# Optimization experiments

Hardware: AMD Instinct MI355X
Metric: run time of the kernel (lower is better)

The kernel has to match this reference:

```python
import jax, jax.numpy as jnp
import numpy as np

U, I, H, E = 50000, 50000, 128, 800000


def segment_softmax(vals, seg, num):
    m = jax.ops.segment_max(vals, seg, num_segments=num)
    ex = jnp.exp(vals - m[seg])
    s = jax.ops.segment_sum(ex, seg, num_segments=num)
    return ex / s[seg]


def setup_inputs() -> dict:
    key = jax.random.key(0)
    ks = jax.random.split(key, 16)
    scale = 1.0 / np.sqrt(H)
    inp = {
        "u_emb": jax.random.normal(ks[0], (U, H), jnp.float32),
        "i_emb": jax.random.normal(ks[1], (I, H), jnp.float32),
        "pVui": jax.random.normal(ks[2], (E, H), jnp.float32),
        "pKiu": jax.random.normal(ks[3], (E, H), jnp.float32),
        "w1": jax.random.normal(ks[4], (H, H), jnp.float32) * scale,
        "w2": jax.random.normal(ks[5], (H, H), jnp.float32) * scale,
        "w1b": jax.random.normal(ks[6], (H, H), jnp.float32) * scale,
        "w2b": jax.random.normal(ks[7], (H, H), jnp.float32) * scale,
        "w3": jax.random.normal(ks[8], (H, H), jnp.float32) * scale,
        "w4": jax.random.normal(ks[9], (H, H), jnp.float32) * scale,
        "edge_index": jax.random.randint(ks[10], (2, E), 0, min(U, I), jnp.int64),
        "last_u": jax.random.randint(ks[11], (2, U), 0, I, jnp.int64),
        "last_i": jax.random.randint(ks[12], (2, I), 0, U, jnp.int64),
        "graph": jnp.zeros((1,), jnp.int64),
    }
    return inp


def reference(u_emb, i_emb, pVui, pKiu, w1, w2, w1b, w2b, w3, w4,
              edge_index, last_u, last_i, graph):
    sqrt_d = np.sqrt(float(u_emb.shape[1])).astype if False else float(np.sqrt(u_emb.shape[1]))
    nu, ni = u_emb.shape[0], i_emb.shape[0]
    src_u, dst_i = edge_index[0], edge_index[1]  # per-edge (user, item)

    # ---- longterm ----
    um_att = u_emb @ w2.T            # [U,H]
    im_att = i_emb @ w1.T            # [I,H]
    # sparse_dense_mul(edge_index, um_att @ im_att.T) -> per-edge dot products
    e_vals = jnp.sum(um_att[src_u] * im_att[dst_i], axis=-1)  # [E]
    e_ui = e_vals + jnp.sum(um_att[src_u] * pVui, axis=-1)
    alphas = segment_softmax(e_ui / sqrt_d, src_u, nu)        # softmax over items per user
    e_iu = e_vals + jnp.sum(im_att[dst_i] * pKiu, axis=-1)
    betas = segment_softmax(e_iu / sqrt_d, dst_i, ni)         # softmax over users per item
    um_b = u_emb @ w2b.T
    im_b = i_emb @ w1b.T
    hLu = jax.ops.segment_sum(alphas[:, None] * (im_b[dst_i] + pKiu), src_u, num_segments=nu)
    hLi = jax.ops.segment_sum(betas[:, None] * (um_b[src_u] + pVui), dst_i, num_segments=ni)

    # ---- shortterm ----
    last_item = i_emb[last_u[1]] @ w3.T   # [U,H] last item embedding per user
    last_user = u_emb[last_i[1]] @ w4.T   # [I,H] last user embedding per item
    a_vals = jnp.sum(last_item[src_u] * im_att[dst_i], axis=-1)
    s_alphas = segment_softmax(a_vals / sqrt_d, src_u, nu)
    b_vals = jnp.sum(last_user[src_u] * im_att[dst_i], axis=-1)
    s_betas = segment_softmax(b_vals / sqrt_d, dst_i, ni)
    # pass_messages with p = ones -> messages + 1
    hSu = jax.ops.segment_sum(s_alphas[:, None] * (im_att[dst_i] + 1.0), src_u, num_segments=nu)
    hSi = jax.ops.segment_sum(s_betas[:, None] * (um_att[src_u] + 1.0), dst_i, num_segments=ni)
    return (hLu, hSu, hLi, hSi)
```

## Files before the change

### kernel.cpp

```cpp
#include <hip/hip_runtime.h>
#include <hip/hip_bf16.h>
#include <math.h>


#define WB 1024

typedef float fvec4 __attribute__((ext_vector_type(4)));

__device__ __forceinline__ float4 nt_load4(const float* p) {
    fvec4 v = __builtin_nontemporal_load((const fvec4*)p);
    return make_float4(v.x, v.y, v.z, v.w);
}
__device__ __forceinline__ float dot4(float4 a, float4 b) {
    return a.x * b.x + a.y * b.y + a.z * b.z + a.w * b.w;
}

struct Gemm6Desc {
    const float* X[6];
    const float* W[6];
    float*       O[6];
    const int*   g[6];
    int          ostride[6];
    int          nrows[6];
};

__global__ __launch_bounds__(256) void gemm6_kernel(Gemm6Desc d)
{
    __shared__ float Xl[64 * 32];
    __shared__ float Wl[128 * 32];
    const int j6 = blockIdx.y;
    const float* __restrict__ X = d.X[j6];
    const float* __restrict__ W = d.W[j6];
    float* __restrict__ O       = d.O[j6];
    const int* __restrict__ gidx = d.g[j6];
    const int ostride = d.ostride[j6];
    const int nrows   = d.nrows[j6];

    const int t  = threadIdx.x;
    const int tx = t & 15;
    const int ty = t >> 4;
    const int brow = blockIdx.x * 64;
    if (brow >= nrows) return;

    float acc[4][8];
#pragma unroll
    for (int j = 0; j < 4; ++j)
#pragma unroll
        for (int i = 0; i < 8; ++i) acc[j][i] = 0.f;

    for (int k0 = 0; k0 < 128; k0 += 32) {
        __syncthreads();
#pragma unroll
        for (int u = 0; u < 2; ++u) {
            int idx4 = t + u * 256;
            int r  = idx4 >> 3;
            int k4 = idx4 & 7;
            int row = brow + r;
            float4 v = make_float4(0.f, 0.f, 0.f, 0.f);
            if (row < nrows) {
                int g = gidx ? gidx[row] : row;
                v = *(const float4*)(X + (size_t)g * 128 + k0 + k4 * 4);
            }
            int sw = k4 ^ ((r >> 3) & 7);
            *(float4*)(Xl + r * 32 + sw * 4) = v;
        }
#pragma unroll
        for (int u = 0; u < 4; ++u) {
            int idx4 = t + u * 256;
            int c  = idx4 >> 3;
            int k4 = idx4 & 7;
            float4 v = *(const float4*)(W + (size_t)c * 128 + k0 + k4 * 4);
            int sw = k4 ^ ((c >> 3) & 7);
            *(float4*)(Wl + c * 32 + sw * 4) = v;
        }
        __syncthreads();
#pragma unroll
        for (int k4 = 0; k4 < 8; ++k4) {
            float4 xv[4], wv[8];
#pragma unroll
            for (int j = 0; j < 4; ++j) {
                int r = ty * 4 + j;
                xv[j] = *(const float4*)(Xl + r * 32 + ((k4 ^ ((r >> 3) & 7)) * 4));
            }
#pragma unroll
            for (int i = 0; i < 8; ++i) {
                int c = tx * 8 + i;
                wv[i] = *(const float4*)(Wl + c * 32 + ((k4 ^ ((c >> 3) & 7)) * 4));
            }
#pragma unroll
            for (int j = 0; j < 4; ++j)
#pragma unroll
                for (int i = 0; i < 8; ++i) {
                    acc[j][i] += xv[j].x * wv[i].x;
                    acc[j][i] += xv[j].y * wv[i].y;
                    acc[j][i] += xv[j].z * wv[i].z;
                    acc[j][i] += xv[j].w * wv[i].w;
                }
        }
    }
#pragma unroll
    for (int j = 0; j < 4; ++j) {
        int row = brow + ty * 4 + j;
        if (row < nrows) {
            float* op = O + (size_t)row * ostride + tx * 8;
            *(float4*)(op)     = make_float4(acc[j][0], acc[j][1], acc[j][2], acc[j][3]);
            *(float4*)(op + 4) = make_float4(acc[j][4], acc[j][5], acc[j][6], acc[j][7]);
        }
    }
}

__global__ __launch_bounds__(256) void hist_kernel(
    const int* __restrict__ ei, int E,
    int* __restrict__ deg_u, int* __restrict__ deg_i)
{
    int e = blockIdx.x * 256 + threadIdx.x;
    if (e < E) {
        atomicAdd(&deg_u[ei[e]], 1);
        atomicAdd(&deg_i[ei[E + e]], 1);
    }
}

__global__ __launch_bounds__(256) void scan_blocksums_kernel(
    const int* __restrict__ deg_u, int nu, int nbu,
    const int* __restrict__ deg_i, int ni,
    int* __restrict__ bsum)
{
    int b = blockIdx.x;
    const int* deg; int n; int base;
    if (b < nbu) { deg = deg_u; n = nu; base = b * WB; }
    else         { deg = deg_i; n = ni; base = (b - nbu) * WB; }
    int t = threadIdx.x;
    int s = 0;
#pragma unroll
    for (int j = 0; j < 4; ++j) {
        int i = base + t * 4 + j;
        if (i < n) s += deg[i];
    }
#pragma unroll
    for (int o = 32; o > 0; o >>= 1) s += __shfl_xor(s, o);
    __shared__ int wt[4];
    if ((t & 63) == 0) wt[t >> 6] = s;
    __syncthreads();
    if (t == 0) bsum[b] = wt[0] + wt[1] + wt[2] + wt[3];
}

__global__ void scan_partials_kernel(
    const int* __restrict__ bsum, int* __restrict__ bscan,
    int nbu, int nbi,
    int* __restrict__ off_u, int nu, int* __restrict__ off_i, int ni)
{
    if (threadIdx.x != 0) return;
    if (blockIdx.x == 0) {
        int c = 0;
        for (int b = 0; b < nbu; ++b) { bscan[b] = c; c += bsum[b]; }
        off_u[nu] = c;
    } else {
        int c = 0;
        for (int b = 0; b < nbi; ++b) { bscan[nbu + b] = c; c += bsum[nbu + b]; }
        off_i[ni] = c;
    }
}

__global__ __launch_bounds__(256) void scan_final_kernel(
    const int* __restrict__ deg_u, int nu, int nbu,
    const int* __restrict__ deg_i, int ni,
    const int* __restrict__ bscan,
    int* __restrict__ off_u, int* __restrict__ cur_u,
    int* __restrict__ off_i, int* __restrict__ cur_i)
{
    int b = blockIdx.x;
    const int* deg; int n; int base; int* off; int* cur;
    if (b < nbu) { deg = deg_u; n = nu; base = b * WB; off = off_u; cur = cur_u; }
    else         { deg = deg_i; n = ni; base = (b - nbu) * WB; off = off_i; cur = cur_i; }
    int t = threadIdx.x;
    int lane = t & 63, w = t >> 6;
    int v[4];
    int s = 0;
#pragma unroll
    for (int j = 0; j < 4; ++j) {
        int i = base + t * 4 + j;
        v[j] = (i < n) ? deg[i] : 0;
        s += v[j];
    }
    int inc = s;
#pragma unroll
    for (int o = 1; o < 64; o <<= 1) {
        int x = __shfl_up(inc, o);
        if (lane >= o) inc += x;
    }
    int excl = inc - s;
    __shared__ int wt[4];
    if (lane == 63) wt[w] = inc;
    __syncthreads();
    int wbase = 0;
    for (int j = 0; j < w; ++j) wbase += wt[j];
    int e = bscan[b] + wbase + excl;
#pragma unroll
    for (int j = 0; j < 4; ++j) {
        int i = base + t * 4 + j;
        if (i < n) { off[i] = e; cur[i] = e; }
        e += v[j];
    }
}

__global__ __launch_bounds__(256) void scatter_ids_kernel(
    const int* __restrict__ ei, int E,
    int* __restrict__ cur_u, int* __restrict__ cur_i,
    int* __restrict__ eu_list, int* __restrict__ ei_list)
{
    int e = blockIdx.x * 256 + threadIdx.x;
    if (e < E) {
        int pu = atomicAdd(&cur_u[ei[e]], 1);
        eu_list[pu] = e;
        int pi = atomicAdd(&cur_i[ei[E + e]], 1);
        ei_list[pi] = e;
    }
}

__global__ __launch_bounds__(256) void gather_u_kernel(
    const float* __restrict__ fusedU,
    const float* __restrict__ fusedI,
    const float* __restrict__ last_item, const float* __restrict__ last_user,
    const float* __restrict__ pVui, const float* __restrict__ pKiu,
    const int* __restrict__ ei, int E,
    const int* __restrict__ off_u, const int* __restrict__ eu_list,
    float2* __restrict__ x24,
    float* __restrict__ hLu, float* __restrict__ hSu, int U, float inv_sqrt_d)
{
    const int wid  = (int)(((size_t)blockIdx.x * blockDim.x + threadIdx.x) >> 6);
    const int lane = threadIdx.x & 63;
    if (wid >= U) return;
    const int g = lane >> 4;
    const int q = lane & 15;

    const float4* fu4 = (const float4*)(fusedU    + (size_t)wid * 256);
    const float4* li4 = (const float4*)(last_item + (size_t)wid * 128);
    const float4* lu4 = (const float4*)(last_user + (size_t)wid * 128);
    const float4 um0 = fu4[q],      um1 = fu4[q + 16];
    const float4 li0 = li4[q],      li1 = li4[q + 16];
    const float4 lu0 = lu4[q],      lu1 = lu4[q + 16];

    float4 a1l = make_float4(0.f,0.f,0.f,0.f), a1h = make_float4(0.f,0.f,0.f,0.f);
    float4 a3l = make_float4(0.f,0.f,0.f,0.f), a3h = make_float4(0.f,0.f,0.f,0.f);
    float s1 = 0.f, s3 = 0.f;
    const int e0 = off_u[wid], e1 = off_u[wid + 1];
    for (int e = e0 + g; e < e1; e += 4) {
        const int eid = eu_list[e];
        const int dst = ei[E + eid];
        const float4* fI = (const float4*)(fusedI + (size_t)dst * 256);
        const float* pvp = pVui + (size_t)eid * 128;
        const float* pkp = pKiu + (size_t)eid * 128;
        float4 ia0 = fI[q],      ia1 = fI[q + 16];
        float4 ib0 = fI[32 + q], ib1 = fI[48 + q];
        float4 pv0 = nt_load4(pvp + q * 4), pv1 = nt_load4(pvp + 64 + q * 4);
        float4 pk0 = nt_load4(pkp + q * 4), pk1 = nt_load4(pkp + 64 + q * 4);

        float p0 = dot4(um0, ia0) + dot4(um1, ia1);
        float p1 = dot4(um0, pv0) + dot4(um1, pv1);
        float p2 = dot4(ia0, pk0) + dot4(ia1, pk1);
        float q1 = p0 + p1;
        float q2 = p0 + p2;
        float q3 = dot4(li0, ia0) + dot4(li1, ia1);
        float q4 = dot4(lu0, ia0) + dot4(lu1, ia1);
#pragma unroll
        for (int o = 8; o > 0; o >>= 1) {
            q1 += __shfl_xor(q1, o);
            q2 += __shfl_xor(q2, o);
            q3 += __shfl_xor(q3, o);
            q4 += __shfl_xor(q4, o);
        }
        float x1 = __expf(q1 * inv_sqrt_d);
        float x2 = __expf(q2 * inv_sqrt_d);
        float x3 = __expf(q3 * inv_sqrt_d);
        float x4 = __expf(q4 * inv_sqrt_d);
        a1l.x += x1*(ib0.x+pk0.x); a1l.y += x1*(ib0.y+pk0.y);
        a1l.z += x1*(ib0.z+pk0.z); a1l.w += x1*(ib0.w+pk0.w);
        a1h.x += x1*(ib1.x+pk1.x); a1h.y += x1*(ib1.y+pk1.y);
        a1h.z += x1*(ib1.z+pk1.z); a1h.w += x1*(ib1.w+pk1.w);
        a3l.x += x3*(ia0.x+1.f);   a3l.y += x3*(ia0.y+1.f);
        a3l.z += x3*(ia0.z+1.f);   a3l.w += x3*(ia0.w+1.f);
        a3h.x += x3*(ia1.x+1.f);   a3h.y += x3*(ia1.y+1.f);
        a3h.z += x3*(ia1.z+1.f);   a3h.w += x3*(ia1.w+1.f);
        s1 += x1; s3 += x3;
        if (q == 0) x24[eid] = make_float2(x2, x4);
    }
#pragma unroll
    for (int o = 16; o <= 32; o <<= 1) {
        a1l.x += __shfl_xor(a1l.x, o); a1l.y += __shfl_xor(a1l.y, o);
        a1l.z += __shfl_xor(a1l.z, o); a1l.w += __shfl_xor(a1l.w, o);
        a1h.x += __shfl_xor(a1h.x, o); a1h.y += __shfl_xor(a1h.y, o);
        a1h.z += __shfl_xor(a1h.z, o); a1h.w += __shfl_xor(a1h.w, o);
        a3l.x += __shfl_xor(a3l.x, o); a3l.y += __shfl_xor(a3l.y, o);
        a3l.z += __shfl_xor(a3l.z, o); a3l.w += __shfl_xor(a3l.w, o);
        a3h.x += __shfl_xor(a3h.x, o); a3h.y += __shfl_xor(a3h.y, o);
        a3h.z += __shfl_xor(a3h.z, o); a3h.w += __shfl_xor(a3h.w, o);
        s1 += __shfl_xor(s1, o);       s3 += __shfl_xor(s3, o);
    }
    if (lane < 16) {
        float r1 = (s1 > 0.f) ? 1.f / s1 : 0.f;
        float r3 = (s3 > 0.f) ? 1.f / s3 : 0.f;
        float4* oL = (float4*)(hLu + (size_t)wid * 128);
        float4* oS = (float4*)(hSu + (size_t)wid * 128);
        oL[q]      = make_float4(a1l.x*r1, a1l.y*r1, a1l.z*r1, a1l.w*r1);
        oL[q + 16] = make_float4(a1h.x*r1, a1h.y*r1, a1h.z*r1, a1h.w*r1);
        oS[q]      = make_float4(a3l.x*r3, a3l.y*r3, a3l.z*r3, a3l.w*r3);
        oS[q + 16] = make_float4(a3h.x*r3, a3h.y*r3, a3h.z*r3, a3h.w*r3);
    }
}

__global__ __launch_bounds__(256) void gather_i_kernel(
    const float* __restrict__ fusedU,
    const float* __restrict__ pVui,
    const int* __restrict__ ei, int E,
    const int* __restrict__ off_i, const int* __restrict__ ei_list,
    const float2* __restrict__ x24,
    float* __restrict__ hLi, float* __restrict__ hSi, int I)
{
    const int wid  = (int)(((size_t)blockIdx.x * blockDim.x + threadIdx.x) >> 6);
    const int lane = threadIdx.x & 63;
    if (wid >= I) return;
    const int g = lane >> 4;
    const int q = lane & 15;

    float4 a2l = make_float4(0.f,0.f,0.f,0.f), a2h = make_float4(0.f,0.f,0.f,0.f);
    float4 a4l = make_float4(0.f,0.f,0.f,0.f), a4h = make_float4(0.f,0.f,0.f,0.f);
    float s2 = 0.f, s4 = 0.f;
    const int e0 = off_i[wid], e1 = off_i[wid + 1];
    for (int e = e0 + g; e < e1; e += 4) {
        const int eid = ei_list[e];
        const int src = ei[eid];
        const float2 x = x24[eid];
        const float4* fU = (const float4*)(fusedU + (size_t)src * 256);
        const float* pvp = pVui + (size_t)eid * 128;
        float4 ua0 = fU[q],      ua1 = fU[q + 16];
        float4 ub0 = fU[32 + q], ub1 = fU[48 + q];
        float4 pv0 = nt_load4(pvp + q * 4), pv1 = nt_load4(pvp + 64 + q * 4);
        a2l.x += x.x*(ub0.x+pv0.x); a2l.y += x.x*(ub0.y+pv0.y);
        a2l.z += x.x*(ub0.z+pv0.z); a2l.w += x.x*(ub0.w+pv0.w);
        a2h.x += x.x*(ub1.x+pv1.x); a2h.y += x.x*(ub1.y+pv1.y);
        a2h.z += x.x*(ub1.z+pv1.z); a2h.w += x.x*(ub1.w+pv1.w);
        a4l.x += x.y*(ua0.x+1.f);   a4l.y += x.y*(ua0.y+1.f);
        a4l.z += x.y*(ua0.z+1.f);   a4l.w += x.y*(ua0.w+1.f);
        a4h.x += x.y*(ua1.x+1.f);   a4h.y += x.y*(ua1.y+1.f);
        a4h.z += x.y*(ua1.z+1.f);   a4h.w += x.y*(ua1.w+1.f);
        s2 += x.x; s4 += x.y;
    }
#pragma unroll
    for (int o = 16; o <= 32; o <<= 1) {
        a2l.x += __shfl_xor(a2l.x, o); a2l.y += __shfl_xor(a2l.y, o);
        a2l.z += __shfl_xor(a2l.z, o); a2l.w += __shfl_xor(a2l.w, o);
        a2h.x += __shfl_xor(a2h.x, o); a2h.y += __shfl_xor(a2h.y, o);
        a2h.z += __shfl_xor(a2h.z, o); a2h.w += __shfl_xor(a2h.w, o);
        a4l.x += __shfl_xor(a4l.x, o); a4l.y += __shfl_xor(a4l.y, o);
        a4l.z += __shfl_xor(a4l.z, o); a4l.w += __shfl_xor(a4l.w, o);
        a4h.x += __shfl_xor(a4h.x, o); a4h.y += __shfl_xor(a4h.y, o);
        a4h.z += __shfl_xor(a4h.z, o); a4h.w += __shfl_xor(a4h.w, o);
        s2 += __shfl_xor(s2, o);       s4 += __shfl_xor(s4, o);
    }
    if (lane < 16) {
        float r2 = (s2 > 0.f) ? 1.f / s2 : 0.f;
        float r4 = (s4 > 0.f) ? 1.f / s4 : 0.f;
        float4* oL = (float4*)(hLi + (size_t)wid * 128);
        float4* oS = (float4*)(hSi + (size_t)wid * 128);
        oL[q]      = make_float4(a2l.x*r2, a2l.y*r2, a2l.z*r2, a2l.w*r2);
        oL[q + 16] = make_float4(a2h.x*r2, a2h.y*r2, a2h.z*r2, a2h.w*r2);
        oS[q]      = make_float4(a4l.x*r4, a4l.y*r4, a4l.z*r4, a4l.w*r4);
        oS[q + 16] = make_float4(a4h.x*r4, a4h.y*r4, a4h.z*r4, a4h.w*r4);
    }
}

extern "C" void kernel_launch(void* const* d_in, const int* in_sizes, int n_in,
                              void* d_out, int out_size, void* d_ws, size_t ws_size,
                              hipStream_t stream)
{
    const float* u_emb = (const float*)d_in[0];
    const float* i_emb = (const float*)d_in[1];
    const float* pVui  = (const float*)d_in[2];
    const float* pKiu  = (const float*)d_in[3];
    const float* w1    = (const float*)d_in[4];
    const float* w2    = (const float*)d_in[5];
    const float* w1b   = (const float*)d_in[6];
    const float* w2b   = (const float*)d_in[7];
    const float* w3    = (const float*)d_in[8];
    const float* w4    = (const float*)d_in[9];
    const int* edge_index = (const int*)d_in[10];
    const int* last_u     = (const int*)d_in[11];
    const int* last_i     = (const int*)d_in[12];

    const int U = in_sizes[0] / 128;
    const int I = in_sizes[1] / 128;
    const int E = in_sizes[10] / 2;
    const int nbu = (U + WB - 1) / WB;
    const int nbi = (I + WB - 1) / WB;

    float* ws = (float*)d_ws;
    float* fusedU    = ws;  ws += (size_t)U * 256;
    float* fusedI    = ws;  ws += (size_t)I * 256;
    float* last_item = ws;  ws += (size_t)U * 128;
    float* last_user = ws;  ws += (size_t)I * 128;
    float2* x24 = (float2*)ws;  ws += (size_t)E * 2;
    int* ip = (int*)ws;
    int* deg_u   = ip;  ip += U;
    int* deg_i   = ip;  ip += I;
    int* off_u   = ip;  ip += U + 1;
    int* off_i   = ip;  ip += I + 1;
    int* cur_u   = ip;  ip += U;
    int* cur_i   = ip;  ip += I;
    int* eu_list = ip;  ip += E;
    int* ei_list = ip;  ip += E;
    int* bsum    = ip;  ip += nbu + nbi;
    int* bscan   = ip;  ip += nbu + nbi;

    float* hLu = (float*)d_out;
    float* hSu = hLu + (size_t)U * 128;
    float* hLi = hSu + (size_t)U * 128;
    float* hSi = hLi + (size_t)I * 128;

    hipMemsetAsync(deg_u, 0, (size_t)(U + I) * sizeof(int), stream);

    dim3 blk(256);
    const int eblk = (E + 255) / 256;
    hist_kernel<<<eblk, blk, 0, stream>>>(edge_index, E, deg_u, deg_i);
    scan_blocksums_kernel<<<nbu + nbi, blk, 0, stream>>>(deg_u, U, nbu, deg_i, I, bsum);
    scan_partials_kernel<<<2, 64, 0, stream>>>(bsum, bscan, nbu, nbi, off_u, U, off_i, I);
    scan_final_kernel<<<nbu + nbi, blk, 0, stream>>>(
        deg_u, U, nbu, deg_i, I, bscan, off_u, cur_u, off_i, cur_i);
    scatter_ids_kernel<<<eblk, blk, 0, stream>>>(edge_index, E, cur_u, cur_i, eu_list, ei_list);

    Gemm6Desc gd;
    gd.X[0] = u_emb; gd.W[0] = w2;  gd.O[0] = fusedU;       gd.g[0] = nullptr;    gd.ostride[0] = 256; gd.nrows[0] = U;
    gd.X[1] = u_emb; gd.W[1] = w2b; gd.O[1] = fusedU + 128; gd.g[1] = nullptr;    gd.ostride[1] = 256; gd.nrows[1] = U;
    gd.X[2] = i_emb; gd.W[2] = w1;  gd.O[2] = fusedI;       gd.g[2] = nullptr;    gd.ostride[2] = 256; gd.nrows[2] = I;
    gd.X[3] = i_emb; gd.W[3] = w1b; gd.O[3] = fusedI + 128; gd.g[3] = nullptr;    gd.ostride[3] = 256; gd.nrows[3] = I;
    gd.X[4] = i_emb; gd.W[4] = w3;  gd.O[4] = last_item;    gd.g[4] = last_u + U; gd.ostride[4] = 128; gd.nrows[4] = U;
    gd.X[5] = u_emb; gd.W[5] = w4;  gd.O[5] = last_user;    gd.g[5] = last_i + I; gd.ostride[5] = 128; gd.nrows[5] = I;
    int maxrows = (U > I) ? U : I;
    dim3 ggrid((maxrows + 63) / 64, 6);
    gemm6_kernel<<<ggrid, blk, 0, stream>>>(gd);

    const float inv_sqrt_d = 1.0f / sqrtf(128.0f);
    gather_u_kernel<<<(U + 3) / 4, blk, 0, stream>>>(
        fusedU, fusedI, last_item, last_user, pVui, pKiu, edge_index, E,
        off_u, eu_list, x24, hLu, hSu, U, inv_sqrt_d);
    gather_i_kernel<<<(I + 3) / 4, blk, 0, stream>>>(
        fusedU, pVui, edge_index, E, off_i, ei_list, x24, hLi, hSi, I);
}
```

Measured before the change: 859.5 us.

## Pack neighbor and edge ids in CSR lists and unroll gather loops two-wide with prefetch

```diff
diff --git a/kernel.cpp b/kernel.cpp
--- a/kernel.cpp
+++ b/kernel.cpp
@@ -206,14 +206,15 @@
 __global__ __launch_bounds__(256) void scatter_ids_kernel(
     const int* __restrict__ ei, int E,
     int* __restrict__ cur_u, int* __restrict__ cur_i,
-    int* __restrict__ eu_list, int* __restrict__ ei_list)
+    int2* __restrict__ eu_list, int2* __restrict__ ei_list)
 {
     int e = blockIdx.x * 256 + threadIdx.x;
     if (e < E) {
-        int pu = atomicAdd(&cur_u[ei[e]], 1);
-        eu_list[pu] = e;
-        int pi = atomicAdd(&cur_i[ei[E + e]], 1);
-        ei_list[pi] = e;
+        int u = ei[e], v = ei[E + e];
+        int pu = atomicAdd(&cur_u[u], 1);
+        eu_list[pu] = make_int2(v, e);
+        int pi = atomicAdd(&cur_i[v], 1);
+        ei_list[pi] = make_int2(u, e);
     }
 }
 
@@ -222,8 +223,8 @@
     const float* __restrict__ fusedI,
     const float* __restrict__ last_item, const float* __restrict__ last_user,
     const float* __restrict__ pVui, const float* __restrict__ pKiu,
-    const int* __restrict__ ei, int E,
-    const int* __restrict__ off_u, const int* __restrict__ eu_list,
+    const int2* __restrict__ lst,
+    const int* __restrict__ off_u,
     float2* __restrict__ x24,
     float* __restrict__ hLu, float* __restrict__ hSu, int U, float inv_sqrt_d)
 {
@@ -244,45 +245,83 @@
     float4 a3l = make_float4(0.f,0.f,0.f,0.f), a3h = make_float4(0.f,0.f,0.f,0.f);
     float s1 = 0.f, s3 = 0.f;
     const int e0 = off_u[wid], e1 = off_u[wid + 1];
-    for (int e = e0 + g; e < e1; e += 4) {
-        const int eid = eu_list[e];
-        const int dst = ei[E + eid];
-        const float4* fI = (const float4*)(fusedI + (size_t)dst * 256);
-        const float* pvp = pVui + (size_t)eid * 128;
-        const float* pkp = pKiu + (size_t)eid * 128;
-        float4 ia0 = fI[q],      ia1 = fI[q + 16];
-        float4 ib0 = fI[32 + q], ib1 = fI[48 + q];
-        float4 pv0 = nt_load4(pvp + q * 4), pv1 = nt_load4(pvp + 64 + q * 4);
-        float4 pk0 = nt_load4(pkp + q * 4), pk1 = nt_load4(pkp + 64 + q * 4);
-
-        float p0 = dot4(um0, ia0) + dot4(um1, ia1);
-        float p1 = dot4(um0, pv0) + dot4(um1, pv1);
-        float p2 = dot4(ia0, pk0) + dot4(ia1, pk1);
-        float q1 = p0 + p1;
-        float q2 = p0 + p2;
-        float q3 = dot4(li0, ia0) + dot4(li1, ia1);
-        float q4 = dot4(lu0, ia0) + dot4(lu1, ia1);
+
+    int eA = e0 + g, eB = eA + 4;
+    bool vA = eA < e1, vB = eB < e1;
+    int2 rA = vA ? lst[eA] : make_int2(0, 0);
+    int2 rB = vB ? lst[eB] : rA;
+
+    while (vA) {
+        int eA2 = eA + 8, eB2 = eB + 8;
+        bool vA2 = eA2 < e1, vB2 = eB2 < e1;
+        int2 rA2 = vA2 ? lst[eA2] : make_int2(0, 0);
+        int2 rB2 = vB2 ? lst[eB2] : rA2;
+
+        const float4* fIA = (const float4*)(fusedI + (size_t)rA.x * 256);
+        const float*  pvA = pVui + (size_t)rA.y * 128;
+        const float*  pkA = pKiu + (size_t)rA.y * 128;
+        const float4* fIB = (const float4*)(fusedI + (size_t)rB.x * 256);
+        const float*  pvB = pVui + (size_t)rB.y * 128;
+        const float*  pkB = pKiu + (size_t)rB.y * 128;
+
+        float4 iaA0 = fIA[q],      iaA1 = fIA[q + 16];
+        float4 ibA0 = fIA[32 + q], ibA1 = fIA[48 + q];
+        float4 pvA0 = nt_load4(pvA + q * 4), pvA1 = nt_load4(pvA + 64 + q * 4);
+        float4 pkA0 = nt_load4(pkA + q * 4), pkA1 = nt_load4(pkA + 64 + q * 4);
+        float4 iaB0 = fIB[q],      iaB1 = fIB[q + 16];
+        float4 ibB0 = fIB[32 + q], ibB1 = fIB[48 + q];
+        float4 pvB0 = nt_load4(pvB + q * 4), pvB1 = nt_load4(pvB + 64 + q * 4);
+        float4 pkB0 = nt_load4(pkB + q * 4), pkB1 = nt_load4(pkB + 64 + q * 4);
+
+        float pA0 = dot4(um0, iaA0) + dot4(um1, iaA1);
+        float qA1 = pA0 + dot4(um0, pvA0) + dot4(um1, pvA1);
+        float qA2 = pA0 + dot4(iaA0, pkA0) + dot4(iaA1, pkA1);
+        float qA3 = dot4(li0, iaA0) + dot4(li1, iaA1);
+        float qA4 = dot4(lu0, iaA0) + dot4(lu1, iaA1);
+        float pB0 = dot4(um0, iaB0) + dot4(um1, iaB1);
+        float qB1 = pB0 + dot4(um0, pvB0) + dot4(um1, pvB1);
+        float qB2 = pB0 + dot4(iaB0, pkB0) + dot4(iaB1, pkB1);
+        float qB3 = dot4(li0, iaB0) + dot4(li1, iaB1);
+        float qB4 = dot4(lu0, iaB0) + dot4(lu1, iaB1);
 #pragma unroll
         for (int o = 8; o > 0; o >>= 1) {
-            q1 += __shfl_xor(q1, o);
-            q2 += __shfl_xor(q2, o);
-            q3 += __shfl_xor(q3, o);
-            q4 += __shfl_xor(q4, o);
+            qA1 += __shfl_xor(qA1, o); qA2 += __shfl_xor(qA2, o);
+            qA3 += __shfl_xor(qA3, o); qA4 += __shfl_xor(qA4, o);
+            qB1 += __shfl_xor(qB1, o); qB2 += __shfl_xor(qB2, o);
+            qB3 += __shfl_xor(qB3, o); qB4 += __shfl_xor(qB4, o);
         }
-        float x1 = __expf(q1 * inv_sqrt_d);
-        float x2 = __expf(q2 * inv_sqrt_d);
-        float x3 = __expf(q3 * inv_sqrt_d);
-        float x4 = __expf(q4 * inv_sqrt_d);
-        a1l.x += x1*(ib0.x+pk0.x); a1l.y += x1*(ib0.y+pk0.y);
-        a1l.z += x1*(ib0.z+pk0.z); a1l.w += x1*(ib0.w+pk0.w);
-        a1h.x += x1*(ib1.x+pk1.x); a1h.y += x1*(ib1.y+pk1.y);
-        a1h.z += x1*(ib1.z+pk1.z); a1h.w += x1*(ib1.w+pk1.w);
-        a3l.x += x3*(ia0.x+1.f);   a3l.y += x3*(ia0.y+1.f);
-        a3l.z += x3*(ia0.z+1.f);   a3l.w += x3*(ia0.w+1.f);
-        a3h.x += x3*(ia1.x+1.f);   a3h.y += x3*(ia1.y+1.f);
-        a3h.z += x3*(ia1.z+1.f);   a3h.w += x3*(ia1.w+1.f);
-        s1 += x1; s3 += x3;
-        if (q == 0) x24[eid] = make_float2(x2, x4);
+        float x1A = __expf(qA1 * inv_sqrt_d);
+        float x2A = __expf(qA2 * inv_sqrt_d);
+        float x3A = __expf(qA3 * inv_sqrt_d);
+        float x4A = __expf(qA4 * inv_sqrt_d);
+        float mB  = vB ? 1.f : 0.f;
+        float x1B = __expf(qB1 * inv_sqrt_d) * mB;
+        float x2B = __expf(qB2 * inv_sqrt_d);
+        float x3B = __expf(qB3 * inv_sqrt_d) * mB;
+        float x4B = __expf(qB4 * inv_sqrt_d);
+
+        a1l.x += x1A*(ibA0.x+pkA0.x) + x1B*(ibB0.x+pkB0.x);
+        a1l.y += x1A*(ibA0.y+pkA0.y) + x1B*(ibB0.y+pkB0.y);
+        a1l.z += x1A*(ibA0.z+pkA0.z) + x1B*(ibB0.z+pkB0.z);
+        a1l.w += x1A*(ibA0.w+pkA0.w) + x1B*(ibB0.w+pkB0.w);
+        a1h.x += x1A*(ibA1.x+pkA1.x) + x1B*(ibB1.x+pkB1.x);
+        a1h.y += x1A*(ibA1.y+pkA1.y) + x1B*(ibB1.y+pkB1.y);
+        a1h.z += x1A*(ibA1.z+pkA1.z) + x1B*(ibB1.z+pkB1.z);
+        a1h.w += x1A*(ibA1.w+pkA1.w) + x1B*(ibB1.w+pkB1.w);
+        a3l.x += x3A*(iaA0.x+1.f) + x3B*(iaB0.x+1.f);
+        a3l.y += x3A*(iaA0.y+1.f) + x3B*(iaB0.y+1.f);
+        a3l.z += x3A*(iaA0.z+1.f) + x3B*(iaB0.z+1.f);
+        a3l.w += x3A*(iaA0.w+1.f) + x3B*(iaB0.w+1.f);
+        a3h.x += x3A*(iaA1.x+1.f) + x3B*(iaB1.x+1.f);
+        a3h.y += x3A*(iaA1.y+1.f) + x3B*(iaB1.y+1.f);
+        a3h.z += x3A*(iaA1.z+1.f) + x3B*(iaB1.z+1.f);
+        a3h.w += x3A*(iaA1.w+1.f) + x3B*(iaB1.w+1.f);
+        s1 += x1A + x1B; s3 += x3A + x3B;
+        if (q == 0) {
+            x24[rA.y] = make_float2(x2A, x4A);
+            if (vB) x24[rB.y] = make_float2(x2B, x4B);
+        }
+        eA = eA2; eB = eB2; vA = vA2; vB = vB2; rA = rA2; rB = rB2;
     }
 #pragma unroll
     for (int o = 16; o <= 32; o <<= 1) {
@@ -311,8 +350,8 @@
 __global__ __launch_bounds__(256) void gather_i_kernel(
     const float* __restrict__ fusedU,
     const float* __restrict__ pVui,
-    const int* __restrict__ ei, int E,
-    const int* __restrict__ off_i, const int* __restrict__ ei_list,
+    const int2* __restrict__ lst,
+    const int* __restrict__ off_i,
     const float2* __restrict__ x24,
     float* __restrict__ hLi, float* __restrict__ hSi, int I)
 {
@@ -326,24 +365,52 @@
     float4 a4l = make_float4(0.f,0.f,0.f,0.f), a4h = make_float4(0.f,0.f,0.f,0.f);
     float s2 = 0.f, s4 = 0.f;
     const int e0 = off_i[wid], e1 = off_i[wid + 1];
-    for (int e = e0 + g; e < e1; e += 4) {
-        const int eid = ei_list[e];
-        const int src = ei[eid];
-        const float2 x = x24[eid];
-        const float4* fU = (const float4*)(fusedU + (size_t)src * 256);
-        const float* pvp = pVui + (size_t)eid * 128;
-        float4 ua0 = fU[q],      ua1 = fU[q + 16];
-        float4 ub0 = fU[32 + q], ub1 = fU[48 + q];
-        float4 pv0 = nt_load4(pvp + q * 4), pv1 = nt_load4(pvp + 64 + q * 4);
-        a2l.x += x.x*(ub0.x+pv0.x); a2l.y += x.x*(ub0.y+pv0.y);
-        a2l.z += x.x*(ub0.z+pv0.z); a2l.w += x.x*(ub0.w+pv0.w);
-        a2h.x += x.x*(ub1.x+pv1.x); a2h.y += x.x*(ub1.y+pv1.y);
-        a2h.z += x.x*(ub1.z+pv1.z); a2h.w += x.x*(ub1.w+pv1.w);
-        a4l.x += x.y*(ua0.x+1.f);   a4l.y += x.y*(ua0.y+1.f);
-        a4l.z += x.y*(ua0.z+1.f);   a4l.w += x.y*(ua0.w+1.f);
-        a4h.x += x.y*(ua1.x+1.f);   a4h.y += x.y*(ua1.y+1.f);
-        a4h.z += x.y*(ua1.z+1.f);   a4h.w += x.y*(ua1.w+1.f);
-        s2 += x.x; s4 += x.y;
+
+    int eA = e0 + g, eB = eA + 4;
+    bool vA = eA < e1, vB = eB < e1;
+    int2 rA = vA ? lst[eA] : make_int2(0, 0);
+    int2 rB = vB ? lst[eB] : rA;
+
+    while (vA) {
+        int eA2 = eA + 8, eB2 = eB + 8;
+        bool vA2 = eA2 < e1, vB2 = eB2 < e1;
+        int2 rA2 = vA2 ? lst[eA2] : make_int2(0, 0);
+        int2 rB2 = vB2 ? lst[eB2] : rA2;
+
+        const float4* fUA = (const float4*)(fusedU + (size_t)rA.x * 256);
+        const float*  pvA = pVui + (size_t)rA.y * 128;
+        const float4* fUB = (const float4*)(fusedU + (size_t)rB.x * 256);
+        const float*  pvB = pVui + (size_t)rB.y * 128;
+
+        float2 xA = x24[rA.y];
+        float2 xB = x24[rB.y];
+        float4 uaA0 = fUA[q],      uaA1 = fUA[q + 16];
+        float4 ubA0 = fUA[32 + q], ubA1 = fUA[48 + q];
+        float4 pvA0 = nt_load4(pvA + q * 4), pvA1 = nt_load4(pvA + 64 + q * 4);
+        float4 uaB0 = fUB[q],      uaB1 = fUB[q + 16];
+        float4 ubB0 = fUB[32 + q], ubB1 = fUB[48 + q];
+        float4 pvB0 = nt_load4(pvB + q * 4), pvB1 = nt_load4(pvB + 64 + q * 4);
+
+        if (!vB) { xB.x = 0.f; xB.y = 0.f; }
+        a2l.x += xA.x*(ubA0.x+pvA0.x) + xB.x*(ubB0.x+pvB0.x);
+        a2l.y += xA.x*(ubA0.y+pvA0.y) + xB.x*(ubB0.y+pvB0.y);
+        a2l.z += xA.x*(ubA0.z+pvA0.z) + xB.x*(ubB0.z+pvB0.z);
+        a2l.w += xA.x*(ubA0.w+pvA0.w) + xB.x*(ubB0.w+pvB0.w);
+        a2h.x += xA.x*(ubA1.x+pvA1.x) + xB.x*(ubB1.x+pvB1.x);
+        a2h.y += xA.x*(ubA1.y+pvA1.y) + xB.x*(ubB1.y+pvB1.y);
+        a2h.z += xA.x*(ubA1.z+pvA1.z) + xB.x*(ubB1.z+pvB1.z);
+        a2h.w += xA.x*(ubA1.w+pvA1.w) + xB.x*(ubB1.w+pvB1.w);
+        a4l.x += xA.y*(uaA0.x+1.f) + xB.y*(uaB0.x+1.f);
+        a4l.y += xA.y*(uaA0.y+1.f) + xB.y*(uaB0.y+1.f);
+        a4l.z += xA.y*(uaA0.z+1.f) + xB.y*(uaB0.z+1.f);
+        a4l.w += xA.y*(uaA0.w+1.f) + xB.y*(uaB0.w+1.f);
+        a4h.x += xA.y*(uaA1.x+1.f) + xB.y*(uaB1.x+1.f);
+        a4h.y += xA.y*(uaA1.y+1.f) + xB.y*(uaB1.y+1.f);
+        a4h.z += xA.y*(uaA1.z+1.f) + xB.y*(uaB1.z+1.f);
+        a4h.w += xA.y*(uaA1.w+1.f) + xB.y*(uaB1.w+1.f);
+        s2 += xA.x + xB.x; s4 += xA.y + xB.y;
+
+        eA = eA2; eB = eB2; vA = vA2; vB = vB2; rA = rA2; rB = rB2;
     }
 #pragma unroll
     for (int o = 16; o <= 32; o <<= 1) {
@@ -354,7 +421,7 @@
         a4l.x += __shfl_xor(a4l.x, o); a4l.y += __shfl_xor(a4l.y, o);
         a4l.z += __shfl_xor(a4l.z, o); a4l.w += __shfl_xor(a4l.w, o);
         a4h.x += __shfl_xor(a4h.x, o); a4h.y += __shfl_xor(a4h.y, o);
-        a4h.z += __shfl_xor(a4h.z, o); a4h.w += __shfl_xor(a4h.w, o);
+        a4h.z += __shfl_xor(a4h.w - a4h.w + a4h.z, o); a4h.w += __shfl_xor(a4h.w, o);
         s2 += __shfl_xor(s2, o);       s4 += __shfl_xor(s4, o);
     }
     if (lane < 16) {
@@ -399,6 +466,8 @@
     float* last_item = ws;  ws += (size_t)U * 128;
     float* last_user = ws;  ws += (size_t)I * 128;
     float2* x24 = (float2*)ws;  ws += (size_t)E * 2;
+    int2* eu_list = (int2*)ws;  ws += (size_t)E * 2;
+    int2* ei_list = (int2*)ws;  ws += (size_t)E * 2;
     int* ip = (int*)ws;
     int* deg_u   = ip;  ip += U;
     int* deg_i   = ip;  ip += I;
@@ -406,8 +475,6 @@
     int* off_i   = ip;  ip += I + 1;
     int* cur_u   = ip;  ip += U;
     int* cur_i   = ip;  ip += I;
-    int* eu_list = ip;  ip += E;
-    int* ei_list = ip;  ip += E;
     int* bsum    = ip;  ip += nbu + nbi;
     int* bscan   = ip;  ip += nbu + nbi;
 
@@ -440,8 +507,8 @@
 
     const float inv_sqrt_d = 1.0f / sqrtf(128.0f);
     gather_u_kernel<<<(U + 3) / 4, blk, 0, stream>>>(
-        fusedU, fusedI, last_item, last_user, pVui, pKiu, edge_index, E,
-        off_u, eu_list, x24, hLu, hSu, U, inv_sqrt_d);
+        fusedU, fusedI, last_item, last_user, pVui, pKiu, eu_list,
+        off_u, x24, hLu, hSu, U, inv_sqrt_d);
     gather_i_kernel<<<(I + 3) / 4, blk, 0, stream>>>(
-        fusedU, pVui, edge_index, E, off_i, ei_list, x24, hLi, hSi, I);
-}
+        fusedU, pVui, ei_list, off_i, x24, hLi, hSi, I);
+}
```

Result: faster. 838.4 us (-2.4%).
